# Kernel tuning notes

Measured on AMD Instinct MI355X. Metric: run time of the kernel, lower is better.

The kernel has to match this reference:

```python
import jax, jax.numpy as jnp
import numpy as np

B = 65536      # total rows = env_batch(8192) * n_slave(8)
DIN = 256      # input_shape
H = 64         # slave_hidden_dim
A = 32         # attention_dim
NACT = 14      # n_actions
NS = 8         # n_slave


def setup_inputs() -> dict:
    key = jax.random.key(0)
    ks = jax.random.split(key, 12)
    s = 0.05
    return {
        "obs": jax.random.normal(ks[0], (B, DIN), jnp.float32),
        "hidden_state": jax.random.normal(ks[1], (B, H), jnp.float32),
        "enc_W": jax.random.normal(ks[2], (DIN, H), jnp.float32) * s,
        "enc_b": jnp.zeros((H,), jnp.float32),
        "gru_Wih": jax.random.normal(ks[3], (3 * H, H), jnp.float32) * s,
        "gru_Whh": jax.random.normal(ks[4], (3 * H, H), jnp.float32) * s,
        "gru_bih": jnp.zeros((3 * H,), jnp.float32),
        "gru_bhh": jnp.zeros((3 * H,), jnp.float32),
        "qW": jax.random.normal(ks[5], (H, A), jnp.float32) * s,
        "kW": jax.random.normal(ks[6], (H, A), jnp.float32) * s,
        "vW": jax.random.normal(ks[7], (H, A), jnp.float32) * s,
        "vb": jnp.zeros((A,), jnp.float32),
        "decW": jax.random.normal(ks[8], (H + A, NACT), jnp.float32) * s,
        "decb": jnp.zeros((NACT,), jnp.float32),
        "n_slave": NS,
    }


def reference(obs, hidden_state, enc_W, enc_b, gru_Wih, gru_Whh, gru_bih, gru_bhh,
              qW, kW, vW, vb, decW, decb, n_slave):
    # encoding + ReLU
    x = jax.nn.relu(obs @ enc_W + enc_b)                      # [B, H]
    # torch GRUCell: r,z,n gate order in weight rows
    gx = x @ gru_Wih.T + gru_bih                              # [B, 3H]
    gh = hidden_state @ gru_Whh.T + gru_bhh                   # [B, 3H]
    xr, xz, xn = jnp.split(gx, 3, axis=-1)
    hr, hz, hn = jnp.split(gh, 3, axis=-1)
    r = jax.nn.sigmoid(xr + hr)
    z = jax.nn.sigmoid(xz + hz)
    n = jnp.tanh(xn + r * hn)
    h_out = (1.0 - z) * n + z * hidden_state                  # [B, H]

    Ad = qW.shape[-1]
    q = (h_out @ qW).reshape(-1, n_slave, Ad)                 # [b, n, A]
    k = (h_out @ kW).reshape(-1, n_slave, Ad)
    v = jax.nn.relu(h_out @ vW + vb).reshape(-1, n_slave, Ad)

    # exclude-self attention == diagonal-masked softmax attention
    scores = jnp.einsum('bia,bja->bij', q, k) / jnp.sqrt(jnp.float32(Ad))
    eye = jnp.eye(n_slave, dtype=bool)
    scores = jnp.where(eye, jnp.float32(-1e9), scores)
    attn = jax.nn.softmax(scores, axis=-1)                    # [b, n, n]
    xatt = jnp.einsum('bij,bja->bia', attn, v).reshape(-1, Ad)  # [B, A]

    out = jnp.concatenate([h_out, xatt], axis=-1) @ decW + decb  # [B, n_actions]
    return (out, h_out)
```

## Files before the change

kernel.cpp:

```cpp
#include <hip/hip_runtime.h>


#define NACT 14
#define BTOT 65536

typedef unsigned int  u32;
typedef unsigned short u16;
using short8 = __attribute__((ext_vector_type(8))) short;
using f32x4  = __attribute__((ext_vector_type(4))) float;

#define ENCB 0
#define WIHB 16896
#define WHHB 30720
#define QKVB 44544
#define DECB 51456
#define WTOT 53120

__device__ u16   g_wbuf[WTOT];
__device__ float g_bias[256];

__device__ __forceinline__ u32 f2bf_rne(float f){
  u32 x = __float_as_uint(f);
  return (x + 0x7fffu + ((x >> 16) & 1u)) >> 16;
}
__device__ __forceinline__ u32 pk2(float a, float b){
  u32 d;
  asm("v_cvt_pk_bf16_f32 %0, %1, %2" : "=v"(d) : "v"(a), "v"(b));
  return d;
}
__device__ __forceinline__ float blo(u32 u){ return __uint_as_float(u << 16); }
__device__ __forceinline__ float bhi(u32 u){ return __uint_as_float(u & 0xffff0000u); }
__device__ __forceinline__ float sigm(float x){ return 1.0f / (1.0f + __expf(-x)); }
__device__ __forceinline__ float tanhp(float x){ return 1.0f - 2.0f / (__expf(2.0f * x) + 1.0f); }
__device__ __forceinline__ short8 as_s8(uint4 v){ union { uint4 u; short8 s; } x; x.u = v; return x.s; }

#define MFMA16(a,b,c) __builtin_amdgcn_mfma_f32_16x16x32_bf16((a),(b),(c),0,0,0)

__global__ void prep(const float* __restrict__ encW, const float* __restrict__ Wih,
                     const float* __restrict__ Whh,  const float* __restrict__ qW,
                     const float* __restrict__ kW,   const float* __restrict__ vW,
                     const float* __restrict__ decW, const float* __restrict__ bih,
                     const float* __restrict__ bhh)
{
  int i = blockIdx.x * 256 + threadIdx.x;
  if (blockIdx.x == 0) {
    int n = threadIdx.x & 63, g = threadIdx.x >> 6;
    float v;
    if      (g == 0) v = bih[n]       + bhh[n];
    else if (g == 1) v = bih[64 + n]  + bhh[64 + n];
    else if (g == 2) v = bih[128 + n];
    else             v = bhh[128 + n];
    g_bias[threadIdx.x] = v;
  }
  if (i >= WTOT) return;
  float val = 0.f;
  if (i < WIHB)      { int n = i / 264, k = i % 264;            if (k < 256) val = encW[k * 64 + n]; }
  else if (i < WHHB) { int j = i - WIHB; int n = j / 72, k = j % 72; if (k < 64) val = Wih[n * 64 + k]; }
  else if (i < QKVB) { int j = i - WHHB; int n = j / 72, k = j % 72; if (k < 64) val = Whh[n * 64 + k]; }
  else if (i < DECB) { int j = i - QKVB; int n = j / 72, k = j % 72;
    if (k < 64) { int m = n >> 5, nn = n & 31;
      val = (m == 0) ? qW[k * 32 + nn] * 0.17677669529663687f
          : (m == 1) ? kW[k * 32 + nn] : vW[k * 32 + nn]; } }
  else { int j = i - DECB; int n = j / 104, k = j % 104; if (n < 14 && k < 96) val = decW[k * 14 + n]; }
  g_wbuf[i] = (u16)f2bf_rne(val);
}

__global__ __launch_bounds__(128, 4)
void commslave_main(const float* __restrict__ obs,  const float* __restrict__ hid,
                    const float* __restrict__ encb, const float* __restrict__ vb,
                    const float* __restrict__ decb, float* __restrict__ out)
{
  __shared__ __align__(16) u16 ldsU[8960];

  const int tid  = threadIdx.x;
  const int lane = tid & 63;
  const int w    = tid >> 6;
  const int quad = lane >> 4;
  const int l16  = lane & 15;
  const int M0   = 16 * w;
  const int gr   = blockIdx.x * 32 + M0;
  float* Sf = (float*)(ldsU + 4608) + w * (16 * 68);

  #pragma unroll
  for (int i = 0; i < 4; i++) {
    int c = lane + 64 * i;
    int lr = c >> 4, c4 = c & 15;
    float4 v = ((const float4*)hid)[(size_t)(gr + lr) * 16 + c4];
    *(uint2*)&ldsU[2304 + (M0 + lr) * 72 + c4 * 4] = make_uint2(pk2(v.x, v.y), pk2(v.z, v.w));
  }

  f32x4 ce[4];
  #pragma unroll
  for (int t = 0; t < 4; t++) { float bv = encb[16 * t + l16]; ce[t] = (f32x4){bv, bv, bv, bv}; }
  #pragma unroll
  for (int ks = 0; ks < 8; ks++) {
    const float* ap = obs + (size_t)(gr + l16) * 256 + ks * 32 + quad * 8;
    float4 a0 = *(const float4*)ap, a1 = *(const float4*)(ap + 4);
    short8 a = as_s8(make_uint4(pk2(a0.x, a0.y), pk2(a0.z, a0.w), pk2(a1.x, a1.y), pk2(a1.z, a1.w)));
    #pragma unroll
    for (int t = 0; t < 4; t++) {
      short8 b = as_s8(*(const uint4*)&g_wbuf[ENCB + (16 * t + l16) * 264 + ks * 32 + quad * 8]);
      ce[t] = MFMA16(a, b, ce[t]);
    }
  }
  #pragma unroll
  for (int t = 0; t < 4; t++)
    #pragma unroll
    for (int r = 0; r < 4; r++)
      Sf[(quad * 4 + r) * 68 + 16 * t + l16] = fmaxf(ce[t][r], 0.f);
  #pragma unroll
  for (int i = 0; i < 2; i++) {
    int c = lane + 64 * i, lr = c >> 3, j = c & 7;
    const float* sp = &Sf[lr * 68 + 8 * j];
    float4 v0 = *(const float4*)sp, v1 = *(const float4*)(sp + 4);
    *(uint4*)&ldsU[(M0 + lr) * 72 + 8 * j] =
        make_uint4(pk2(v0.x, v0.y), pk2(v0.z, v0.w), pk2(v1.x, v1.y), pk2(v1.z, v1.w));
  }
  __syncthreads();

  short8 ax[2], ah[2];
  #pragma unroll
  for (int ks = 0; ks < 2; ks++) {
    ax[ks] = *(const short8*)&ldsU[(M0 + l16) * 72 + ks * 32 + quad * 8];
    ah[ks] = *(const short8*)&ldsU[2304 + (M0 + l16) * 72 + ks * 32 + quad * 8];
  }
  #pragma unroll
  for (int u = 0; u < 4; u++) {
    f32x4 g6[6];
    #pragma unroll
    for (int t = 0; t < 6; t++) g6[t] = (f32x4){0.f, 0.f, 0.f, 0.f};
    #pragma unroll
    for (int g = 0; g < 3; g++) {
      int row = 64 * g + 16 * u + l16;
      #pragma unroll
      for (int ks = 0; ks < 2; ks++) {
        short8 bi = as_s8(*(const uint4*)&g_wbuf[WIHB + row * 72 + ks * 32 + quad * 8]);
        g6[g] = MFMA16(ax[ks], bi, g6[g]);
        short8 bh = as_s8(*(const uint4*)&g_wbuf[WHHB + row * 72 + ks * 32 + quad * 8]);
        g6[3 + g] = MFMA16(ah[ks], bh, g6[3 + g]);
      }
    }
    int nc = 16 * u + l16;
    float brz = g_bias[nc], bzz = g_bias[64 + nc], bni = g_bias[128 + nc], bnh = g_bias[192 + nc];
    #pragma unroll
    for (int r = 0; r < 4; r++) {
      float hp = blo(ldsU[2304 + (M0 + quad * 4 + r) * 72 + nc]);
      float rg = sigm(g6[0][r] + g6[3][r] + brz);
      float zg = sigm(g6[1][r] + g6[4][r] + bzz);
      float nn = tanhp(g6[2][r] + bni + rg * (g6[5][r] + bnh));
      Sf[(quad * 4 + r) * 68 + nc] = (1.f - zg) * nn + zg * hp;
    }
  }
  #pragma unroll
  for (int i = 0; i < 2; i++) {
    int c = lane + 64 * i, lr = c >> 3, j = c & 7;
    const float* sp = &Sf[lr * 68 + 8 * j];
    float4 v0 = *(const float4*)sp, v1 = *(const float4*)(sp + 4);
    *(uint4*)&ldsU[2304 + (M0 + lr) * 72 + 8 * j] =
        make_uint4(pk2(v0.x, v0.y), pk2(v0.z, v0.w), pk2(v1.x, v1.y), pk2(v1.z, v1.w));
  }
  __syncthreads();

  short8 hx[2];
  #pragma unroll
  for (int ks = 0; ks < 2; ks++)
    hx[ks] = *(const short8*)&ldsU[2304 + (M0 + l16) * 72 + ks * 32 + quad * 8];
  f32x4 cq[6];
  #pragma unroll
  for (int t = 0; t < 6; t++) {
    float bv = (t >= 4) ? vb[16 * (t - 4) + l16] : 0.f;
    cq[t] = (f32x4){bv, bv, bv, bv};
  }
  #pragma unroll
  for (int ks = 0; ks < 2; ks++)
    #pragma unroll
    for (int t = 0; t < 6; t++) {
      short8 b = as_s8(*(const uint4*)&g_wbuf[QKVB + (16 * t + l16) * 72 + ks * 32 + quad * 8]);
      cq[t] = MFMA16(hx[ks], b, cq[t]);
    }
  #pragma unroll
  for (int t = 0; t < 4; t++)
    #pragma unroll
    for (int r = 0; r < 4; r++)
      Sf[(quad * 4 + r) * 68 + 16 * t + l16] = cq[t][r];
  #pragma unroll
  for (int t = 4; t < 6; t++)
    #pragma unroll
    for (int r = 0; r < 4; r++)
      ldsU[(M0 + quad * 4 + r) * 72 + 32 + 16 * (t - 4) + l16] =
          (u16)pk2(fmaxf(cq[t][r], 0.f), 0.f);
  __syncthreads();

  {
    const int r_l = lane >> 2, s4 = lane & 3;
    const int gb = r_l & 8, ri = r_l & 7;
    const float* fq = &Sf[r_l * 68];
    float sc[2];
    #pragma unroll
    for (int jj = 0; jj < 2; jj++) {
      int j = s4 + 4 * jj;
      const float* fk = &Sf[(gb + j) * 68 + 32];
      float d = 0.f;
      #pragma unroll
      for (int a4 = 0; a4 < 32; a4 += 4) {
        float4 q4 = *(const float4*)&fq[a4];
        float4 k4 = *(const float4*)&fk[a4];
        d += q4.x * k4.x + q4.y * k4.y + q4.z * k4.z + q4.w * k4.w;
      }
      sc[jj] = (j == ri) ? -1e30f : d;
    }
    float m = fmaxf(sc[0], sc[1]);
    m = fmaxf(m, __shfl_xor(m, 1));
    m = fmaxf(m, __shfl_xor(m, 2));
    float p0 = (s4     == ri) ? 0.f : __expf(sc[0] - m);
    float p1 = (s4 + 4 == ri) ? 0.f : __expf(sc[1] - m);
    float sum = p0 + p1;
    sum += __shfl_xor(sum, 1);
    sum += __shfl_xor(sum, 2);
    float inv = 1.f / sum;
    Sf[r_l * 68 + s4]     = p0 * inv;
    Sf[r_l * 68 + 4 + s4] = p1 * inv;
    float xa[8] = {0, 0, 0, 0, 0, 0, 0, 0};
    #pragma unroll
    for (int j = 0; j < 8; j++) {
      float aj = Sf[r_l * 68 + j];
      uint4 uv = *(const uint4*)&ldsU[(M0 + gb + j) * 72 + 32 + 8 * s4];
      xa[0] += aj * blo(uv.x); xa[1] += aj * bhi(uv.x);
      xa[2] += aj * blo(uv.y); xa[3] += aj * bhi(uv.y);
      xa[4] += aj * blo(uv.z); xa[5] += aj * bhi(uv.z);
      xa[6] += aj * blo(uv.w); xa[7] += aj * bhi(uv.w);
    }
    *(uint4*)&ldsU[(M0 + r_l) * 72 + 8 * s4] =
        make_uint4(pk2(xa[0], xa[1]), pk2(xa[2], xa[3]), pk2(xa[4], xa[5]), pk2(xa[6], xa[7]));
  }
  __syncthreads();

  {
    float db = (l16 < NACT) ? decb[l16] : 0.f;
    f32x4 co = (f32x4){db, db, db, db};
    #pragma unroll
    for (int ks = 0; ks < 2; ks++) {
      short8 a = *(const short8*)&ldsU[2304 + (M0 + l16) * 72 + ks * 32 + quad * 8];
      short8 b = as_s8(*(const uint4*)&g_wbuf[DECB + l16 * 104 + ks * 32 + quad * 8]);
      co = MFMA16(a, b, co);
    }
    short8 a2 = *(const short8*)&ldsU[(M0 + l16) * 72 + quad * 8];
    short8 b2 = as_s8(*(const uint4*)&g_wbuf[DECB + l16 * 104 + 64 + quad * 8]);
    co = MFMA16(a2, b2, co);
    if (l16 < NACT) {
      #pragma unroll
      for (int r = 0; r < 4; r++)
        out[(size_t)(gr + quad * 4 + r) * NACT + l16] = co[r];
    }
  }

  {
    float* outH = out + (size_t)BTOT * NACT;
    #pragma unroll
    for (int i = 0; i < 2; i++) {
      int c = lane + 64 * i, lr = c >> 3, j = c & 7;
      uint4 u = *(const uint4*)&ldsU[2304 + (M0 + lr) * 72 + 8 * j];
      *(float4*)(outH + (size_t)(gr + lr) * 64 + 8 * j) =
          make_float4(blo(u.x), bhi(u.x), blo(u.y), bhi(u.y));
      *(float4*)(outH + (size_t)(gr + lr) * 64 + 8 * j + 4) =
          make_float4(blo(u.z), bhi(u.z), blo(u.w), bhi(u.w));
    }
  }
}

extern "C" void kernel_launch(void* const* d_in, const int* in_sizes, int n_in,
                              void* d_out, int out_size, void* d_ws, size_t ws_size,
                              hipStream_t stream) {
  (void)in_sizes; (void)n_in; (void)d_ws; (void)ws_size; (void)out_size;
  const float* obs  = (const float*)d_in[0];
  const float* hid  = (const float*)d_in[1];
  const float* encW = (const float*)d_in[2];
  const float* encb = (const float*)d_in[3];
  const float* Wih  = (const float*)d_in[4];
  const float* Whh  = (const float*)d_in[5];
  const float* bih  = (const float*)d_in[6];
  const float* bhh  = (const float*)d_in[7];
  const float* qW   = (const float*)d_in[8];
  const float* kW   = (const float*)d_in[9];
  const float* vW   = (const float*)d_in[10];
  const float* vb   = (const float*)d_in[11];
  const float* decW = (const float*)d_in[12];
  const float* decb = (const float*)d_in[13];
  float* out = (float*)d_out;

  prep<<<(WTOT + 255) / 256, 256, 0, stream>>>(encW, Wih, Whh, qW, kW, vW, decW, bih, bhh);
  commslave_main<<<BTOT / 32, 128, 0, stream>>>(obs, hid, encb, vb, decb, out);
}
```

Before: 163.7 us.

## Process two 16-row M-tiles per wave to reuse weight fragments

Each wave now handles 32 rows instead of 16, so every weight fragment loaded from global memory feeds two MFMAs, for the encoder, GRU, QKV and decoder GEMMs. Block row count doubles, LDS doubles, the grid halves and launch bounds drop to 2 waves-per-EU. The attention step is remapped to 2 lanes per row with 4 scores each. The aim is to halve weight-load traffic per row, at the cost of more registers, lower occupancy and fewer blocks for latency hiding.

```diff
diff --git a/kernel.cpp b/kernel.cpp
--- a/kernel.cpp
+++ b/kernel.cpp
@@ -65,51 +65,62 @@
   g_wbuf[i] = (u16)f2bf_rne(val);
 }
 
-__global__ __launch_bounds__(128, 4)
+__global__ __launch_bounds__(128, 2)
 void commslave_main(const float* __restrict__ obs,  const float* __restrict__ hid,
                     const float* __restrict__ encb, const float* __restrict__ vb,
                     const float* __restrict__ decb, float* __restrict__ out)
 {
-  __shared__ __align__(16) u16 ldsU[8960];
+  __shared__ __align__(16) u16 ldsU[17920];
 
   const int tid  = threadIdx.x;
   const int lane = tid & 63;
   const int w    = tid >> 6;
   const int quad = lane >> 4;
   const int l16  = lane & 15;
-  const int M0   = 16 * w;
-  const int gr   = blockIdx.x * 32 + M0;
-  float* Sf = (float*)(ldsU + 4608) + w * (16 * 68);
-
-  #pragma unroll
-  for (int i = 0; i < 4; i++) {
+  const int M0   = 32 * w;
+  const int gr   = blockIdx.x * 64 + M0;
+  float* Sf = (float*)(ldsU + 9216) + w * (32 * 68);
+
+  #pragma unroll
+  for (int i = 0; i < 8; i++) {
     int c = lane + 64 * i;
     int lr = c >> 4, c4 = c & 15;
     float4 v = ((const float4*)hid)[(size_t)(gr + lr) * 16 + c4];
-    *(uint2*)&ldsU[2304 + (M0 + lr) * 72 + c4 * 4] = make_uint2(pk2(v.x, v.y), pk2(v.z, v.w));
-  }
-
-  f32x4 ce[4];
-  #pragma unroll
-  for (int t = 0; t < 4; t++) { float bv = encb[16 * t + l16]; ce[t] = (f32x4){bv, bv, bv, bv}; }
+    *(uint2*)&ldsU[4608 + (M0 + lr) * 72 + c4 * 4] = make_uint2(pk2(v.x, v.y), pk2(v.z, v.w));
+  }
+
+  f32x4 ce[2][4];
+  #pragma unroll
+  for (int t = 0; t < 4; t++) {
+    float bv = encb[16 * t + l16];
+    ce[0][t] = (f32x4){bv, bv, bv, bv};
+    ce[1][t] = (f32x4){bv, bv, bv, bv};
+  }
   #pragma unroll
   for (int ks = 0; ks < 8; ks++) {
-    const float* ap = obs + (size_t)(gr + l16) * 256 + ks * 32 + quad * 8;
-    float4 a0 = *(const float4*)ap, a1 = *(const float4*)(ap + 4);
-    short8 a = as_s8(make_uint4(pk2(a0.x, a0.y), pk2(a0.z, a0.w), pk2(a1.x, a1.y), pk2(a1.z, a1.w)));
+    short8 a[2];
+    #pragma unroll
+    for (int mt = 0; mt < 2; mt++) {
+      const float* ap = obs + (size_t)(gr + 16 * mt + l16) * 256 + ks * 32 + quad * 8;
+      float4 a0 = *(const float4*)ap, a1 = *(const float4*)(ap + 4);
+      a[mt] = as_s8(make_uint4(pk2(a0.x, a0.y), pk2(a0.z, a0.w), pk2(a1.x, a1.y), pk2(a1.z, a1.w)));
+    }
     #pragma unroll
     for (int t = 0; t < 4; t++) {
       short8 b = as_s8(*(const uint4*)&g_wbuf[ENCB + (16 * t + l16) * 264 + ks * 32 + quad * 8]);
-      ce[t] = MFMA16(a, b, ce[t]);
-    }
-  }
-  #pragma unroll
-  for (int t = 0; t < 4; t++)
-    #pragma unroll
-    for (int r = 0; r < 4; r++)
-      Sf[(quad * 4 + r) * 68 + 16 * t + l16] = fmaxf(ce[t][r], 0.f);
-  #pragma unroll
-  for (int i = 0; i < 2; i++) {
+      ce[0][t] = MFMA16(a[0], b, ce[0][t]);
+      ce[1][t] = MFMA16(a[1], b, ce[1][t]);
+    }
+  }
+  #pragma unroll
+  for (int mt = 0; mt < 2; mt++)
+    #pragma unroll
+    for (int t = 0; t < 4; t++)
+      #pragma unroll
+      for (int r = 0; r < 4; r++)
+        Sf[(16 * mt + quad * 4 + r) * 68 + 16 * t + l16] = fmaxf(ce[mt][t][r], 0.f);
+  #pragma unroll
+  for (int i = 0; i < 4; i++) {
     int c = lane + 64 * i, lr = c >> 3, j = c & 7;
     const float* sp = &Sf[lr * 68 + 8 * j];
     float4 v0 = *(const float4*)sp, v1 = *(const float4*)(sp + 4);
@@ -118,87 +129,104 @@
   }
   __syncthreads();
 
-  short8 ax[2], ah[2];
-  #pragma unroll
-  for (int ks = 0; ks < 2; ks++) {
-    ax[ks] = *(const short8*)&ldsU[(M0 + l16) * 72 + ks * 32 + quad * 8];
-    ah[ks] = *(const short8*)&ldsU[2304 + (M0 + l16) * 72 + ks * 32 + quad * 8];
-  }
-  #pragma unroll
+  short8 ax[2][2], ah[2][2];
+  #pragma unroll
+  for (int mt = 0; mt < 2; mt++)
+    #pragma unroll
+    for (int ks = 0; ks < 2; ks++) {
+      ax[mt][ks] = *(const short8*)&ldsU[(M0 + 16 * mt + l16) * 72 + ks * 32 + quad * 8];
+      ah[mt][ks] = *(const short8*)&ldsU[4608 + (M0 + 16 * mt + l16) * 72 + ks * 32 + quad * 8];
+    }
+  #pragma unroll 1
   for (int u = 0; u < 4; u++) {
-    f32x4 g6[6];
-    #pragma unroll
-    for (int t = 0; t < 6; t++) g6[t] = (f32x4){0.f, 0.f, 0.f, 0.f};
+    f32x4 g6[2][6];
+    #pragma unroll
+    for (int mt = 0; mt < 2; mt++)
+      #pragma unroll
+      for (int t = 0; t < 6; t++) g6[mt][t] = (f32x4){0.f, 0.f, 0.f, 0.f};
     #pragma unroll
     for (int g = 0; g < 3; g++) {
       int row = 64 * g + 16 * u + l16;
       #pragma unroll
       for (int ks = 0; ks < 2; ks++) {
         short8 bi = as_s8(*(const uint4*)&g_wbuf[WIHB + row * 72 + ks * 32 + quad * 8]);
-        g6[g] = MFMA16(ax[ks], bi, g6[g]);
         short8 bh = as_s8(*(const uint4*)&g_wbuf[WHHB + row * 72 + ks * 32 + quad * 8]);
-        g6[3 + g] = MFMA16(ah[ks], bh, g6[3 + g]);
+        #pragma unroll
+        for (int mt = 0; mt < 2; mt++) {
+          g6[mt][g]     = MFMA16(ax[mt][ks], bi, g6[mt][g]);
+          g6[mt][3 + g] = MFMA16(ah[mt][ks], bh, g6[mt][3 + g]);
+        }
       }
     }
     int nc = 16 * u + l16;
     float brz = g_bias[nc], bzz = g_bias[64 + nc], bni = g_bias[128 + nc], bnh = g_bias[192 + nc];
     #pragma unroll
-    for (int r = 0; r < 4; r++) {
-      float hp = blo(ldsU[2304 + (M0 + quad * 4 + r) * 72 + nc]);
-      float rg = sigm(g6[0][r] + g6[3][r] + brz);
-      float zg = sigm(g6[1][r] + g6[4][r] + bzz);
-      float nn = tanhp(g6[2][r] + bni + rg * (g6[5][r] + bnh));
-      Sf[(quad * 4 + r) * 68 + nc] = (1.f - zg) * nn + zg * hp;
-    }
-  }
-  #pragma unroll
-  for (int i = 0; i < 2; i++) {
+    for (int mt = 0; mt < 2; mt++)
+      #pragma unroll
+      for (int r = 0; r < 4; r++) {
+        int lr = 16 * mt + quad * 4 + r;
+        float hp = blo(ldsU[4608 + (M0 + lr) * 72 + nc]);
+        float rg = sigm(g6[mt][0][r] + g6[mt][3][r] + brz);
+        float zg = sigm(g6[mt][1][r] + g6[mt][4][r] + bzz);
+        float nn = tanhp(g6[mt][2][r] + bni + rg * (g6[mt][5][r] + bnh));
+        Sf[lr * 68 + nc] = (1.f - zg) * nn + zg * hp;
+      }
+  }
+  #pragma unroll
+  for (int i = 0; i < 4; i++) {
     int c = lane + 64 * i, lr = c >> 3, j = c & 7;
     const float* sp = &Sf[lr * 68 + 8 * j];
     float4 v0 = *(const float4*)sp, v1 = *(const float4*)(sp + 4);
-    *(uint4*)&ldsU[2304 + (M0 + lr) * 72 + 8 * j] =
+    *(uint4*)&ldsU[4608 + (M0 + lr) * 72 + 8 * j] =
         make_uint4(pk2(v0.x, v0.y), pk2(v0.z, v0.w), pk2(v1.x, v1.y), pk2(v1.z, v1.w));
   }
   __syncthreads();
 
-  short8 hx[2];
-  #pragma unroll
-  for (int ks = 0; ks < 2; ks++)
-    hx[ks] = *(const short8*)&ldsU[2304 + (M0 + l16) * 72 + ks * 32 + quad * 8];
-  f32x4 cq[6];
+  short8 hx[2][2];
+  #pragma unroll
+  for (int mt = 0; mt < 2; mt++)
+    #pragma unroll
+    for (int ks = 0; ks < 2; ks++)
+      hx[mt][ks] = *(const short8*)&ldsU[4608 + (M0 + 16 * mt + l16) * 72 + ks * 32 + quad * 8];
+  f32x4 cq[2][6];
   #pragma unroll
   for (int t = 0; t < 6; t++) {
     float bv = (t >= 4) ? vb[16 * (t - 4) + l16] : 0.f;
-    cq[t] = (f32x4){bv, bv, bv, bv};
+    cq[0][t] = (f32x4){bv, bv, bv, bv};
+    cq[1][t] = (f32x4){bv, bv, bv, bv};
   }
   #pragma unroll
   for (int ks = 0; ks < 2; ks++)
     #pragma unroll
     for (int t = 0; t < 6; t++) {
       short8 b = as_s8(*(const uint4*)&g_wbuf[QKVB + (16 * t + l16) * 72 + ks * 32 + quad * 8]);
-      cq[t] = MFMA16(hx[ks], b, cq[t]);
-    }
-  #pragma unroll
-  for (int t = 0; t < 4; t++)
-    #pragma unroll
-    for (int r = 0; r < 4; r++)
-      Sf[(quad * 4 + r) * 68 + 16 * t + l16] = cq[t][r];
-  #pragma unroll
-  for (int t = 4; t < 6; t++)
-    #pragma unroll
-    for (int r = 0; r < 4; r++)
-      ldsU[(M0 + quad * 4 + r) * 72 + 32 + 16 * (t - 4) + l16] =
-          (u16)pk2(fmaxf(cq[t][r], 0.f), 0.f);
+      cq[0][t] = MFMA16(hx[0][ks], b, cq[0][t]);
+      cq[1][t] = MFMA16(hx[1][ks], b, cq[1][t]);
+    }
+  #pragma unroll
+  for (int mt = 0; mt < 2; mt++) {
+    #pragma unroll
+    for (int t = 0; t < 4; t++)
+      #pragma unroll
+      for (int r = 0; r < 4; r++)
+        Sf[(16 * mt + quad * 4 + r) * 68 + 16 * t + l16] = cq[mt][t][r];
+    #pragma unroll
+    for (int t = 4; t < 6; t++)
+      #pragma unroll
+      for (int r = 0; r < 4; r++)
+        ldsU[(M0 + 16 * mt + quad * 4 + r) * 72 + 32 + 16 * (t - 4) + l16] =
+            (u16)pk2(fmaxf(cq[mt][t][r], 0.f), 0.f);
+  }
   __syncthreads();
 
   {
-    const int r_l = lane >> 2, s4 = lane & 3;
-    const int gb = r_l & 8, ri = r_l & 7;
+    const int r_l = lane >> 1, s2 = lane & 1;
+    const int gb = r_l & ~7, ri = r_l & 7;
     const float* fq = &Sf[r_l * 68];
-    float sc[2];
-    #pragma unroll
-    for (int jj = 0; jj < 2; jj++) {
-      int j = s4 + 4 * jj;
+    float sc[4];
+    #pragma unroll
+    for (int jj = 0; jj < 4; jj++) {
+      int j = 4 * s2 + jj;
       const float* fk = &Sf[(gb + j) * 68 + 32];
       float d = 0.f;
       #pragma unroll
@@ -209,57 +237,77 @@
       }
       sc[jj] = (j == ri) ? -1e30f : d;
     }
-    float m = fmaxf(sc[0], sc[1]);
+    float m = fmaxf(fmaxf(sc[0], sc[1]), fmaxf(sc[2], sc[3]));
     m = fmaxf(m, __shfl_xor(m, 1));
-    m = fmaxf(m, __shfl_xor(m, 2));
-    float p0 = (s4     == ri) ? 0.f : __expf(sc[0] - m);
-    float p1 = (s4 + 4 == ri) ? 0.f : __expf(sc[1] - m);
-    float sum = p0 + p1;
+    float p[4], sum = 0.f;
+    #pragma unroll
+    for (int jj = 0; jj < 4; jj++) {
+      int j = 4 * s2 + jj;
+      p[jj] = (j == ri) ? 0.f : __expf(sc[jj] - m);
+      sum += p[jj];
+    }
     sum += __shfl_xor(sum, 1);
-    sum += __shfl_xor(sum, 2);
     float inv = 1.f / sum;
-    Sf[r_l * 68 + s4]     = p0 * inv;
-    Sf[r_l * 68 + 4 + s4] = p1 * inv;
-    float xa[8] = {0, 0, 0, 0, 0, 0, 0, 0};
+    #pragma unroll
+    for (int jj = 0; jj < 4; jj++)
+      Sf[r_l * 68 + 4 * s2 + jj] = p[jj] * inv;
+    float xa[16];
+    #pragma unroll
+    for (int u = 0; u < 16; u++) xa[u] = 0.f;
     #pragma unroll
     for (int j = 0; j < 8; j++) {
       float aj = Sf[r_l * 68 + j];
-      uint4 uv = *(const uint4*)&ldsU[(M0 + gb + j) * 72 + 32 + 8 * s4];
-      xa[0] += aj * blo(uv.x); xa[1] += aj * bhi(uv.x);
-      xa[2] += aj * blo(uv.y); xa[3] += aj * bhi(uv.y);
-      xa[4] += aj * blo(uv.z); xa[5] += aj * bhi(uv.z);
-      xa[6] += aj * blo(uv.w); xa[7] += aj * bhi(uv.w);
-    }
-    *(uint4*)&ldsU[(M0 + r_l) * 72 + 8 * s4] =
-        make_uint4(pk2(xa[0], xa[1]), pk2(xa[2], xa[3]), pk2(xa[4], xa[5]), pk2(xa[6], xa[7]));
+      const u16* vp = &ldsU[(M0 + gb + j) * 72 + 32 + 16 * s2];
+      uint4 v0 = *(const uint4*)vp, v1 = *(const uint4*)(vp + 8);
+      xa[0]  += aj * blo(v0.x); xa[1]  += aj * bhi(v0.x);
+      xa[2]  += aj * blo(v0.y); xa[3]  += aj * bhi(v0.y);
+      xa[4]  += aj * blo(v0.z); xa[5]  += aj * bhi(v0.z);
+      xa[6]  += aj * blo(v0.w); xa[7]  += aj * bhi(v0.w);
+      xa[8]  += aj * blo(v1.x); xa[9]  += aj * bhi(v1.x);
+      xa[10] += aj * blo(v1.y); xa[11] += aj * bhi(v1.y);
+      xa[12] += aj * blo(v1.z); xa[13] += aj * bhi(v1.z);
+      xa[14] += aj * blo(v1.w); xa[15] += aj * bhi(v1.w);
+    }
+    u16* xp = &ldsU[(M0 + r_l) * 72 + 16 * s2];
+    *(uint4*)xp = make_uint4(pk2(xa[0], xa[1]), pk2(xa[2], xa[3]),
+                             pk2(xa[4], xa[5]), pk2(xa[6], xa[7]));
+    *(uint4*)(xp + 8) = make_uint4(pk2(xa[8], xa[9]),  pk2(xa[10], xa[11]),
+                                   pk2(xa[12], xa[13]), pk2(xa[14], xa[15]));
   }
   __syncthreads();
 
   {
     float db = (l16 < NACT) ? decb[l16] : 0.f;
-    f32x4 co = (f32x4){db, db, db, db};
+    f32x4 co[2] = {(f32x4){db, db, db, db}, (f32x4){db, db, db, db}};
     #pragma unroll
     for (int ks = 0; ks < 2; ks++) {
-      short8 a = *(const short8*)&ldsU[2304 + (M0 + l16) * 72 + ks * 32 + quad * 8];
       short8 b = as_s8(*(const uint4*)&g_wbuf[DECB + l16 * 104 + ks * 32 + quad * 8]);
-      co = MFMA16(a, b, co);
-    }
-    short8 a2 = *(const short8*)&ldsU[(M0 + l16) * 72 + quad * 8];
+      #pragma unroll
+      for (int mt = 0; mt < 2; mt++) {
+        short8 a = *(const short8*)&ldsU[4608 + (M0 + 16 * mt + l16) * 72 + ks * 32 + quad * 8];
+        co[mt] = MFMA16(a, b, co[mt]);
+      }
+    }
     short8 b2 = as_s8(*(const uint4*)&g_wbuf[DECB + l16 * 104 + 64 + quad * 8]);
-    co = MFMA16(a2, b2, co);
-    if (l16 < NACT) {
-      #pragma unroll
-      for (int r = 0; r < 4; r++)
-        out[(size_t)(gr + quad * 4 + r) * NACT + l16] = co[r];
-    }
+    #pragma unroll
+    for (int mt = 0; mt < 2; mt++) {
+      short8 a2 = *(const short8*)&ldsU[(M0 + 16 * mt + l16) * 72 + quad * 8];
+      co[mt] = MFMA16(a2, b2, co[mt]);
+    }
+    if (l16 < NACT)
+      #pragma unroll
+      for (int mt = 0; mt < 2; mt++)
+        #pragma unroll
+        for (int r = 0; r < 4; r++)
+          out[(size_t)(gr + 16 * mt + quad * 4 + r) * NACT + l16] = co[mt][r];
   }
 
   {
     float* outH = out + (size_t)BTOT * NACT;
     #pragma unroll
-    for (int i = 0; i < 2; i++) {
+    for (int i = 0; i < 4; i++) {
       int c = lane + 64 * i, lr = c >> 3, j = c & 7;
-      uint4 u = *(const uint4*)&ldsU[2304 + (M0 + lr) * 72 + 8 * j];
+      uint4 u = *(const uint4*)&ldsU[4608 + (M0 + lr) * 72 + 8 * j];
       *(float4*)(outH + (size_t)(gr + lr) * 64 + 8 * j) =
           make_float4(blo(u.x), bhi(u.x), blo(u.y), bhi(u.y));
       *(float4*)(outH + (size_t)(gr + lr) * 64 + 8 * j + 4) =
@@ -289,5 +337,5 @@
   float* out = (float*)d_out;
 
   prep<<<(WTOT + 255) / 256, 256, 0, stream>>>(encW, Wih, Whh, qW, kW, vW, decW, bih, bhh);
-  commslave_main<<<BTOT / 32, 128, 0, stream>>>(obs, hid, encb, vb, decb, out);
-}
+  commslave_main<<<BTOT / 64, 128, 0, stream>>>(obs, hid, encb, vb, decb, out);
+}
```

After: 154.2 us. 1.06x faster.
